# Performance work log

Hardware: AMD Instinct MI355X
Metric: run time of the kernel (lower is better)

The kernel has to match this reference:

```python
import jax, jax.numpy as jnp
import numpy as np

B, T, Nt = 64, 256, 77      # batch, motion length, text tokens
H, L = 8, 64                # num_heads, latent_dim per head
D = H * L                   # 512 model dim
Pt = 256                    # text_latent_dim
Ht = 1                      # num_text_heads
E, K = 8, 2                 # num_experts, topk
TEMB = 2048                 # time_embed_dim
MAXS, MAXTS = 512, 77       # max_seq_len, max_text_seq_len
NEG = -1e6


def _ln(x, g, b, eps=1e-5):
    m = jnp.mean(x, -1, keepdims=True)
    v = jnp.mean((x - m) ** 2, -1, keepdims=True)
    return (x - m) * jax.lax.rsqrt(v + eps) * g + b


def _gelu(x):
    return jax.nn.gelu(x, approximate=False)


def _moe_tokens(x, gate_w, fc1w, fc1b, fc2w, fc2b):
    # top-k softmax gate (fp32) + expert FFNs; dense compute, sparse combine.
    logits = x.astype(jnp.float32) @ gate_w.astype(jnp.float32)          # [Ntok,E]
    gates = jax.nn.softmax(logits, axis=-1)
    topv, topi = jax.lax.top_k(gates, K)
    topv = topv / jnp.sum(topv, -1, keepdims=True)
    dense = jnp.sum(jax.nn.one_hot(topi, E, dtype=topv.dtype) * topv[..., None], axis=1)
    dense = dense.astype(x.dtype)                                        # [Ntok,E]
    y = jnp.zeros((x.shape[0], fc2w.shape[-1]), x.dtype)
    for e in range(E):  # small fixed expert loop
        h = _gelu(x @ fc1w[e] + fc1b[e])
        y = y + dense[:, e:e + 1] * (h @ fc2w[e] + fc2b[e])
    return y


def _moe_block(x, pos, gate_w, fc1w, fc1b, fc2w, fc2b, projw, projb):
    # x: [B,Tn,Hn,Din]; add learned positional embedding, MoE over tokens, GELU, proj.
    b, t, h, d = x.shape
    x = x + pos[:, :t]
    y = _moe_tokens(x.reshape(-1, d), gate_w, fc1w, fc1b, fc2w, fc2b)
    y = _gelu(y) @ projw + projb
    return y.reshape(b, t, h, -1)


def _fwd(x, xf, emb, src_mask, norm_g, norm_b, tnorm_g, tnorm_b, m_pos, m_gate, m_fc1w, m_fc1b, m_fc2w, m_fc2b, m_projw, m_projb, t_pos, t_gate, t_fc1w, t_fc1b, t_fc2w, t_fc2b, t_projw, t_projb, body_w, sb_embw, sb_embb, sb_ng, sb_nb, sb_outw, sb_outb, cond_type):
    Bx, Tx, Dx = x.shape
    x4 = x.reshape(Bx, Tx, H, L)
    tf = xf.reshape(Bx, Nt, Ht, Pt)
    text_feat = _moe_block(_ln(tf, tnorm_g, tnorm_b), t_pos, t_gate, t_fc1w, t_fc1b, t_fc2w, t_fc2b, t_projw, t_projb)      # [B,Nt,Ht,2L]
    motion_feat = _moe_block(_ln(x4, norm_g, norm_b), m_pos, m_gate, m_fc1w, m_fc1b, m_fc2w, m_fc2b, m_projw, m_projb)      # [B,T,H,4L]
    # static body-part mixing
    bw = jax.nn.softmax(body_w, axis=1)
    body_feat = jnp.einsum('hl,bnld->bnhd', bw, motion_feat[..., :L]).reshape(Bx, Tx, Dx)
    tc = (cond_type % 10 > 0).astype(x.dtype).reshape(Bx, 1, 1, 1)
    sm = src_mask.reshape(Bx, Tx, 1, 1)
    key_text = jnp.broadcast_to(text_feat[..., :L] + (1.0 - tc) * NEG, (Bx, Nt, H, L))
    key_motion = motion_feat[..., L:2 * L] + (1.0 - sm) * NEG
    key = jax.nn.softmax(jnp.concatenate([key_text, key_motion], axis=1), axis=1)  # softmax over N
    val_text = jnp.broadcast_to(text_feat[..., L:] * tc, (Bx, Nt, H, L))
    val_motion = motion_feat[..., 2 * L:3 * L] * sm
    value = jnp.concatenate([val_text, val_motion], axis=1)                        # [B,N,H,L]
    query = jax.nn.softmax(motion_feat[..., 3 * L:], axis=-1)                      # [B,T,H,L]
    attn = jnp.einsum('bnhd,bnhl->bhdl', key, value)                               # [B,H,L,L]
    y_t = jnp.einsum('bnhd,bhdl->bnhl', query, attn).reshape(Bx, Tx, Dx)
    # StylizationBlock (eval: dropout is identity)
    h = _ln(body_feat + y_t, sb_ng, sb_nb)
    eo = jax.nn.silu(emb) @ sb_embw + sb_embb                                      # [B,2D]
    h = h * (1.0 + eo[:, None, :Dx]) + eo[:, None, Dx:]
    h = jax.nn.silu(h) @ sb_outw + sb_outb
    return x + h


def setup_inputs() -> dict:
    ks = iter(jax.random.split(jax.random.key(0), 48))
    nrm = lambda shape, s: jax.random.normal(next(ks), shape, jnp.float32) * s
    return {
        "x": nrm((B, T, D), 1.0),
        "xf": nrm((B, Nt, Pt), 1.0),
        "emb": nrm((B, TEMB), 1.0),
        "src_mask": jnp.ones((B, T, 1), jnp.float32),
        "norm_g": jnp.ones((L,), jnp.float32), "norm_b": jnp.zeros((L,), jnp.float32),
        "tnorm_g": jnp.ones((Pt,), jnp.float32), "tnorm_b": jnp.zeros((Pt,), jnp.float32),
        "m_pos": nrm((1, MAXS, H, L), 0.02),
        "m_gate": nrm((L, E), 0.02),
        "m_fc1w": nrm((E, L, 4 * L), 0.02), "m_fc1b": jnp.zeros((E, 4 * L), jnp.float32),
        "m_fc2w": nrm((E, 4 * L, L), 0.02), "m_fc2b": jnp.zeros((E, L), jnp.float32),
        "m_projw": nrm((L, 4 * L), 0.02), "m_projb": jnp.zeros((4 * L,), jnp.float32),
        "t_pos": nrm((1, MAXTS, Ht, Pt), 0.02),
        "t_gate": nrm((Pt, E), 0.02),
        "t_fc1w": nrm((E, Pt, 4 * Pt), 0.02), "t_fc1b": jnp.zeros((E, 4 * Pt), jnp.float32),
        "t_fc2w": nrm((E, 4 * Pt, Pt), 0.02), "t_fc2b": jnp.zeros((E, Pt), jnp.float32),
        "t_projw": nrm((Pt, 2 * L), 0.02), "t_projb": jnp.zeros((2 * L,), jnp.float32),
        "body_w": nrm((H, H), 1.0),
        "sb_embw": nrm((TEMB, 2 * D), 0.02), "sb_embb": jnp.zeros((2 * D,), jnp.float32),
        "sb_ng": jnp.ones((D,), jnp.float32), "sb_nb": jnp.zeros((D,), jnp.float32),
        "sb_outw": nrm((D, D), 0.02), "sb_outb": jnp.zeros((D,), jnp.float32),
        "cond_type": jax.random.randint(next(ks), (B, 1, 1), 0, 100, jnp.int32),
        "motion_length": T,
        "num_intervals": 1,
    }


def reference(x, xf, emb, src_mask, norm_g, norm_b, tnorm_g, tnorm_b, m_pos, m_gate, m_fc1w, m_fc1b, m_fc2w, m_fc2b, m_projw, m_projb, t_pos, t_gate, t_fc1w, t_fc1b, t_fc2w, t_fc2b, t_projw, t_projb, body_w, sb_embw, sb_embb, sb_ng, sb_nb, sb_outw, sb_outb, cond_type, motion_length, num_intervals):
    # motion_length / num_intervals are unused by the forward math (as in the source).
    return _fwd(x, xf, emb, src_mask, norm_g, norm_b, tnorm_g, tnorm_b, m_pos, m_gate, m_fc1w, m_fc1b, m_fc2w, m_fc2b, m_projw, m_projb, t_pos, t_gate, t_fc1w, t_fc1b, t_fc2w, t_fc2b, t_projw, t_projb, body_w, sb_embw, sb_embb, sb_ng, sb_nb, sb_outw, sb_outb, cond_type)
```

## Files before the change

### kernel.cpp

```cpp
#include <hip/hip_runtime.h>
#include <hip/hip_bf16.h>


typedef __hip_bfloat16 bf16;
typedef unsigned short u16;
typedef unsigned int   u32;
typedef __attribute__((ext_vector_type(8))) short short8;
typedef __attribute__((ext_vector_type(4))) short s16x4;
typedef __attribute__((ext_vector_type(4))) float f32x4;

#define MFMA16(a,b,c) __builtin_amdgcn_mfma_f32_16x16x32_bf16(a,b,c,0,0,0)

__device__ __forceinline__ float b2f(bf16 v){ return __bfloat162float(v); }
__device__ __forceinline__ u16 f2bu(float f){
  union { __hip_bfloat16 hh; u16 us; } cv; cv.hh = __float2bfloat16(f); return cv.us;
}
__device__ __forceinline__ float bu2f(u16 v){ return __uint_as_float(((u32)v)<<16); }

__device__ __forceinline__ float geluf(float x){
  float t = x*x;
  float w = x * fmaf(-0.10294453f, t, -2.3022077f);
  float z = exp2f(w);
  return x * __builtin_amdgcn_rcpf(1.f + z);
}
__device__ __forceinline__ float siluf(float x){
  float z = exp2f(-1.442695f * x);
  return x * __builtin_amdgcn_rcpf(1.f + z);
}

__device__ __forceinline__ float wsum(float v){
#pragma unroll
  for (int o=32;o>0;o>>=1) v += __shfl_xor(v,o,64);
  return v;
}
__device__ __forceinline__ float wmax(float v){
#pragma unroll
  for (int o=32;o>0;o>>=1) v = fmaxf(v, __shfl_xor(v,o,64));
  return v;
}
__device__ __forceinline__ void top2(const float* lg, int& i1, int& i2, float& wA){
  i1 = 0; float v1 = lg[0];
#pragma unroll
  for (int e=1;e<8;e++) if (lg[e] > v1){ v1 = lg[e]; i1 = e; }
  i2 = 0; float v2 = -1e30f;
#pragma unroll
  for (int e=0;e<8;e++) if (e != i1 && lg[e] > v2){ v2 = lg[e]; i2 = e; }
  wA = 1.f/(1.f + expf(v2 - v1));
}

__device__ __forceinline__ float sum2_wave(float x, int b0){
  float s = x, ss = x*x;
  float v = (b0 ? ss : s) + __shfl_xor(b0 ? s : ss, 1, 64);
  v += __shfl_xor(v, 2, 64);
  v += __shfl_xor(v, 4, 64);
  v += __shfl_xor(v, 8, 64);
  v += __shfl_xor(v, 16, 64);
  v += __shfl_xor(v, 32, 64);
  return v;
}

__device__ __forceinline__ float rsum8(const float p[8], int lane){
  int b0 = lane & 1, b1 = lane & 2, b2 = lane & 4;
  float w[4], u[2], v;
#pragma unroll
  for (int j=0;j<4;j++){
    float keep = b0 ? p[2*j+1] : p[2*j];
    float send = b0 ? p[2*j]   : p[2*j+1];
    w[j] = keep + __shfl_xor(send, 1, 64);
  }
#pragma unroll
// ... 90 lines not shown
  int tok = blockIdx.x, tid = threadIdx.x;
  int n = tok % 77;
  __shared__ float redw[32], lgs[8];
  int w = tid >> 6, ln = tid & 63;
  int b0 = tid & 1;
  float xv = xf[tok*256 + tid];
  float v = sum2_wave(xv, b0);
  if (ln < 2) redw[w*2 + ln] = v;
  __syncthreads();
  float mean = (redw[0]+redw[2]+redw[4]+redw[6]) * (1.f/256.f);
  float var  = (redw[1]+redw[3]+redw[5]+redw[7]) * (1.f/256.f) - mean*mean;
  float r = rsqrtf(var + 1e-5f);
  float xn = (xv - mean)*r*tg[tid] + tb[tid] + tpos[n*256 + tid];
  xtb[tok*256 + tid] = f2bu(xn);
  float p[8];
#pragma unroll
  for (int e=0;e<8;e++) p[e] = xn * gw[tid*8 + e];
  float vv = rsum8(p, ln);
  __syncthreads();
  if (ln < 8) redw[w*8 + ln] = vv;
  __syncthreads();
  if (tid < 8) lgs[tid] = redw[tid] + redw[8+tid] + redw[16+tid] + redw[24+tid];
  __syncthreads();
  if (tid == 0){
    int i1, i2; float wA; top2(lgs, i1, i2, wA);
    eidxT[tok] = make_int2(i1, i2);
    ewT[tok] = make_float2(wA, 1.f - wA);
  }
}

__global__ __launch_bounds__(256) void k_motion_pre(
    const float* __restrict__ x, const float* __restrict__ ng, const float* __restrict__ nb,
    const float* __restrict__ mpos, const float* __restrict__ gw,
    u16* __restrict__ xmb, int2* __restrict__ eidxM, float2* __restrict__ ewM){
  int tok = blockIdx.x*4 + (threadIdx.x >> 6);
  int d = threadIdx.x & 63;
  int b0 = d & 1;
  float xv = x[(size_t)tok*64 + d];
  float v = sum2_wave(xv, b0);
  float o = __shfl_xor(v, 1, 64);
  float sf  = b0 ? o : v;
  float ssf = b0 ? v : o;
  float mean = sf * (1.f/64.f);
  float var  = ssf * (1.f/64.f) - mean*mean;
  float r = rsqrtf(var + 1e-5f);
  int h = tok & 7; int t = (tok >> 3) & 255;
  float xn = (xv - mean)*r*ng[d] + nb[d] + mpos[(t*8+h)*64 + d];
  xmb[(size_t)tok*64 + d] = f2bu(xn);
  float p[8];
#pragma unroll
  for (int e=0;e<8;e++) p[e] = xn * gw[d*8 + e];
  float vv = rsum8(p, d);
  float lg[8];
#pragma unroll
  for (int e=0;e<8;e++) lg[e] = __shfl(vv, e, 64);
  if (d == 0){
    int i1, i2; float wA; top2(lg, i1, i2, wA);
    eidxM[tok] = make_int2(i1, i2);
    ewM[tok] = make_float2(wA, 1.f - wA);
  }
}

__global__ __launch_bounds__(256, 4) void k_motion_moe(
    const u16* __restrict__ xmb, const int* __restrict__ alistM, const int* __restrict__ cnts,
    const u16* __restrict__ w1pk, const float* __restrict__ fc1b,
    const u16* __restrict__ w2pk, const float* __restrict__ fc2b,
    u16* __restrict__ ycM){
  int e = blockIdx.y, tile = blockIdx.x, tid = threadIdx.x;
  int cnt = cnts[8+e]; int base = tile*32;
  if (base >= cnt) return;
  int nn = min(32, cnt - base); int off = e*131072;
  __shared__ int toks[32];
  __shared__ u16 xs[32*72];
  __shared__ u16 hT[32*264];
  if (tid < 32) toks[tid] = alistM[off + base + min(tid, nn-1)];
  __syncthreads();
  { int row = tid >> 3, c0 = (tid & 7)*8;
    short8 v = *(const short8*)(xmb + (size_t)(toks[row]>>1)*64 + c0);
    *(short8*)&xs[row*72 + c0] = v; }
  __syncthreads();
  int lane = tid & 63, w = tid >> 6;
  int n = lane & 15, q = lane >> 4;
  int mt = w & 1;
  short8 x0 = *(const short8*)&xs[(mt*16 + n)*72 + q*8];
  short8 x1 = *(const short8*)&xs[(mt*16 + n)*72 + 32 + q*8];
  const short8* b1 = (const short8*)(w1pk + (size_t)e*16384);
  short8 b1f[16];
#pragma unroll
  for (int i=0;i<8;i++){
    int nt = (w>>1)*8 + i;
    b1f[2*i]   = b1[(nt*2+0)*64 + lane];
    b1f[2*i+1] = b1[(nt*2+1)*64 + lane];
  }
#pragma unroll
  for (int i=0;i<8;i++){
    int nt = (w>>1)*8 + i;
    f32x4 acc = {0.f,0.f,0.f,0.f};
    acc = MFMA16(b1f[2*i],   x0, acc);
    acc = MFMA16(b1f[2*i+1], x1, acc);
    f32x4 bias = *(const f32x4*)(fc1b + e*256 + nt*16 + q*4);
    s16x4 o;
#pragma unroll
    for (int r=0;r<4;r++) o[r] = (short)f2bu(geluf(acc[r] + bias[r]));
    *(s16x4*)&hT[(mt*16 + n)*264 + nt*16 + q*4] = o;
  }
  __syncthreads();
  short8 a2[8];
#pragma unroll
  for (int kc=0;kc<8;kc++) a2[kc] = *(const short8*)&hT[(mt*16 + n)*264 + kc*32 + q*8];
  const short8* b2 = (const short8*)(w2pk + (size_t)e*16384);
  bool valid = (mt*16 + n) < nn;
  int slot = toks[mt*16 + n];
#pragma unroll
  for (int i=0;i<2;i++){
    int nt = (w>>1)*2 + i;
    f32x4 acc = {0.f,0.f,0.f,0.f};
#pragma unroll
    for (int kc=0;kc<8;kc++) acc = MFMA16(b2[(nt*8+kc)*64 + lane], a2[kc], acc);
    f32x4 bias = *(const f32x4*)(fc2b + e*64 + nt*16 + q*4);
    if (valid){
      s16x4 o;
#pragma unroll
      for (int r=0;r<4;r++) o[r] = (short)f2bu(acc[r] + bias[r]);
      *(s16x4*)(ycM + (size_t)slot*64 + nt*16 + q*4) = o;
    }
  }
}

__global__ __launch_bounds__(256) void k_text_moe(
    const u16* __restrict__ xtb, const int* __restrict__ alistT, const int* __restrict__ cnts,
    const u16* __restrict__ w1pk, const float* __restrict__ fc1b,
    const u16* __restrict__ w2pk, const float* __restrict__ fc2b,
    float* __restrict__ ycT){
  int e = blockIdx.y, tile = blockIdx.x, tid = threadIdx.x;
  int cnt = cnts[e]; int base = tile*16;
  if (base >= cnt) return;
  int nn = min(16, cnt - base); int off = e*4928;
  __shared__ int toks[16];
  __shared__ u16 xs[16*280];
  __shared__ u16 hT[16*1048];
  if (tid < 16) toks[tid] = alistT[off + base + min(tid, nn-1)];
  __syncthreads();
  { int row = tid >> 4, c0 = (tid & 15)*16;
    const short8* sp = (const short8*)(xtb + (size_t)(toks[row]>>1)*256 + c0);
    short8 v0 = sp[0], v1 = sp[1];
    *(short8*)&xs[row*280 + c0] = v0;
    *(short8*)&xs[row*280 + c0 + 8] = v1; }
  __syncthreads();
  int lane = tid & 63, w = tid >> 6;
  int n = lane & 15, q = lane >> 4;
  short8 a_[8];
#pragma unroll
  for (int kc=0;kc<8;kc++) a_[kc] = *(const short8*)&xs[n*280 + kc*32 + q*8];
  const short8* b1 = (const short8*)(w1pk + (size_t)e*262144);
#pragma unroll 1
  for (int i=0;i<16;i++){
    int nt = w*16 + i;
// ... 16 lines not shown
#pragma unroll
    for (int i=0;i<4;i++){
      int nt = w*4 + i;
      acc[i] = MFMA16(a, b2[(nt*32+kc)*64 + lane], acc[i]);
    }
  }
#pragma unroll
  for (int i=0;i<4;i++){
    int nt = w*4 + i;
    float bias = fc2b[e*256 + nt*16 + n];
#pragma unroll
    for (int r=0;r<4;r++){
      int row = q*4 + r;
      if (row < nn) ycT[(size_t)toks[row]*256 + nt*16 + n] = acc[i][r] + bias;
    }
  }
}

__global__ __launch_bounds__(128) void k_text_combine(
    const float* __restrict__ ycT, const float2* __restrict__ ewT,
    const float* __restrict__ pw, const float* __restrict__ pb,
    float* __restrict__ tfeat){
  int t = blockIdx.x, tid = threadIdx.x;
  __shared__ float gy[256];
  float2 w = ewT[t];
  for (int c=tid; c<256; c+=128){
    float y = w.x*ycT[(size_t)(t*2)*256 + c] + w.y*ycT[(size_t)(t*2+1)*256 + c];
    gy[c] = geluf(y);
  }
  __syncthreads();
  float a = pb[tid];
  for (int k=0;k<256;k++) a += gy[k] * pw[k*128 + tid];
  tfeat[(size_t)t*128 + tid] = a;
}

__global__ __launch_bounds__(256) void k_mproj(
    const u16* __restrict__ ycM, const float2* __restrict__ ewM,
    const u16* __restrict__ wpk, const float* __restrict__ pb,
    u16* __restrict__ mf, u16* __restrict__ qs){
  int t0 = blockIdx.x*32, tid = threadIdx.x;
  __shared__ u16 xs[32*72];
  { int row = tid >> 3, c0 = (tid & 7)*8;
    int tok = t0 + row;
    float2 wgt = ewM[tok];
    short8 v0 = *(const short8*)(ycM + (size_t)(tok*2)*64 + c0);
    short8 v1 = *(const short8*)(ycM + (size_t)(tok*2+1)*64 + c0);
    short8 o;
#pragma unroll
    for (int j=0;j<8;j++)
      o[j] = (short)f2bu(geluf(wgt.x*bu2f((u16)v0[j]) + wgt.y*bu2f((u16)v1[j])));
    *(short8*)&xs[row*72 + c0] = o; }
  __syncthreads();
  int lane = tid & 63, w = tid >> 6;
  int n = lane & 15, q = lane >> 4;
  int mt = w & 1;
  short8 a0 = *(const short8*)&xs[(mt*16 + n)*72 + q*8];
  short8 a1 = *(const short8*)&xs[(mt*16 + n)*72 + 32 + q*8];
  const short8* bp = (const short8*)wpk;
  float vals[4][4];
#pragma unroll
  for (int i=0;i<8;i++){
    int nt = (w>>1)*8 + i;
    f32x4 acc = {0.f,0.f,0.f,0.f};
    acc = MFMA16(a0, bp[(nt*2+0)*64 + lane], acc);
    acc = MFMA16(a1, bp[(nt*2+1)*64 + lane], acc);
    float bias = pb[nt*16 + n];
#pragma unroll
    for (int r=0;r<4;r++){
      float v = acc[r] + bias;
      if (w >= 2 && i >= 4) vals[i-4][r] = v;
      int tok = t0 + mt*16 + q*4 + r;
      mf[(size_t)tok*256 + nt*16 + n] = f2bu(v);
    }
  }
  if (w >= 2){
#pragma unroll
    for (int r=0;r<4;r++){
      int tok = t0 + mt*16 + q*4 + r;
      float m = fmaxf(fmaxf(vals[0][r], vals[1][r]), fmaxf(vals[2][r], vals[3][r]));
#pragma unroll
      for (int o=8;o>0;o>>=1) m = fmaxf(m, __shfl_xor(m, o, 64));
      float e0 = expf(vals[0][r]-m), e1 = expf(vals[1][r]-m);
      float e2 = expf(vals[2][r]-m), e3 = expf(vals[3][r]-m);
      float s = (e0+e1) + (e2+e3);
#pragma unroll
      for (int o=8;o>0;o>>=1) s += __shfl_xor(s, o, 64);
      float inv = __builtin_amdgcn_rcpf(s);
      u16* qp = qs + (size_t)tok*64 + n;
      qp[0]  = f2bu(e0*inv);
      qp[16] = f2bu(e1*inv);
      qp[32] = f2bu(e2*inv);
      qp[48] = f2bu(e3*inv);
    }
  }
}

__global__ __launch_bounds__(256) void k_eo1(const float* __restrict__ emb, const float* __restrict__ ew,
                      float* __restrict__ ep){
  int ct = blockIdx.x & 15;
  int ks = blockIdx.x >> 4;
  int tid = threadIdx.x;
  int k0 = ks*128, c0 = ct*64;
  __shared__ float aS[128*68];
  __shared__ float bS[128*64];
#pragma unroll
  for (int i=0;i<8;i++){
    int idx4 = tid + i*256;
    int b = idx4 >> 5, kq = idx4 & 31;
    f32x4 v = *(const f32x4*)(emb + (size_t)b*2048 + k0 + kq*4);
    aS[(kq*4+0)*68 + b] = siluf(v[0]);
    aS[(kq*4+1)*68 + b] = siluf(v[1]);
    aS[(kq*4+2)*68 + b] = siluf(v[2]);
    aS[(kq*4+3)*68 + b] = siluf(v[3]);
  }
#pragma unroll
  for (int i=0;i<8;i++){
    int idx4 = tid + i*256;
    int kk = idx4 >> 4, cq = idx4 & 15;
    *(f32x4*)&bS[kk*64 + cq*4] = *(const f32x4*)(ew + (size_t)(k0+kk)*1024 + c0 + cq*4);
  }
  __syncthreads();
  int cg = tid & 15, bg = tid >> 4;
  f32x4 acc[4] = {{0.f,0.f,0.f,0.f},{0.f,0.f,0.f,0.f},{0.f,0.f,0.f,0.f},{0.f,0.f,0.f,0.f}};
#pragma unroll 4
  for (int kk=0;kk<128;kk++){
    f32x4 a = *(const f32x4*)&aS[kk*68 + bg*4];
    f32x4 bb = *(const f32x4*)&bS[kk*64 + cg*4];
#pragma unroll
    for (int i=0;i<4;i++){
      acc[i][0] += a[i]*bb[0];
      acc[i][1] += a[i]*bb[1];
      acc[i][2] += a[i]*bb[2];
      acc[i][3] += a[i]*bb[3];
    }
  }
#pragma unroll
  for (int i=0;i<4;i++){
    int b = bg*4 + i;
    *(f32x4*)&ep[((size_t)(ks*64 + b))*1024 + c0 + cg*4] = acc[i];
  }
}

__global__ __launch_bounds__(256) void k_eo2(const float* __restrict__ ep, const float* __restrict__ ebias,
                      float* __restrict__ eo){
  int idx = blockIdx.x*256 + threadIdx.x;
  int c = idx & 1023;
  float s = ebias[c];
#pragma unroll
  for (int ks=0;ks<16;ks++) s += ep[(size_t)ks*65536 + idx];
  eo[idx] = s;
}

#define AT_STRIDE 364
__global__ __launch_bounds__(512) void k_attn(const float* __restrict__ tfeat, const u16* __restrict__ mf,
                       const float* __restrict__ src_mask, const int* __restrict__ cond,
                       u16* __restrict__ attnT){
  int b = blockIdx.x >> 3; int h = blockIdx.x & 7;
  int tid = threadIdx.x; int c = tid & 63; int part = tid >> 6;
  __shared__ u16 ebT[64*AT_STRIDE];
  __shared__ u16 vbT[64*AT_STRIDE];
  __shared__ float colmax[64], colsum[64], red[512];
  float tc = ((cond[b] % 10) > 0) ? 1.f : 0.f;
  float negt = (1.f - tc) * (-1e6f);

  float mx = -1e30f;
  for (int k = 0; k < 11; k++){
    int n0 = part*44 + k*4;
    s16x4 kb4, vb4;
#pragma unroll
    for (int jj = 0; jj < 4; jj++){
      int n = n0 + jj;
      float kv, vv;
      if (n < 77){
        const float* trow = tfeat + (b*77+n)*128;
        kv = trow[c] + negt;
        vv = trow[64 + c] * tc;
      } else if (n < 333){
        int t = n - 77; float smv = src_mask[b*256 + t];
        const u16* mrow = mf + ((size_t)(b*256+t)*8+h)*256;
        kv = bu2f(mrow[64 + c]) + (1.f - smv)*(-1e6f);
        vv = bu2f(mrow[128 + c]) * smv;
      } else { kv = -1e30f; vv = 0.f; }
      kb4[jj] = (short)f2bu(kv);
      vb4[jj] = (short)f2bu(vv);
      mx = fmaxf(mx, kv);
    }
    *(s16x4*)&ebT[c*AT_STRIDE + n0] = kb4;
    *(s16x4*)&vbT[c*AT_STRIDE + n0] = vb4;
  }
// ... 19 lines not shown
      s16x4 o;
      o[0]=(short)f2bu(e0); o[1]=(short)f2bu(e1); o[2]=(short)f2bu(e2); o[3]=(short)f2bu(e3);
      *(s16x4*)&ebT[rowc*AT_STRIDE + n0] = o;
    }
    red[tid] = s;
  }
  __syncthreads();
  if (tid < 64){
    float t2 = 0.f;
#pragma unroll
    for (int p=0;p<8;p++) t2 += red[tid*8 + p];
    colsum[tid] = t2;
  }
  __syncthreads();
  int lane = tid & 63, w = tid >> 6;
  int n16 = lane & 15, q = lane >> 4;
  int mt = w >> 1;
  int ntb = (w & 1) * 2;
  f32x4 acc0 = {0.f,0.f,0.f,0.f}, acc1 = {0.f,0.f,0.f,0.f};
  const u16* ea = &ebT[(mt*16 + n16)*AT_STRIDE + q*8];
  const u16* v0p = &vbT[(ntb*16 + n16)*AT_STRIDE + q*8];
  const u16* v1p = &vbT[((ntb+1)*16 + n16)*AT_STRIDE + q*8];
#pragma unroll
  for (int kc = 0; kc < 11; kc++){
    short8 a  = ld8(ea  + kc*32);
    short8 b0 = ld8(v0p + kc*32);
    short8 b1 = ld8(v1p + kc*32);
    acc0 = MFMA16(a, b0, acc0);
    acc1 = MFMA16(a, b1, acc1);
  }
  float inv[4];
#pragma unroll
  for (int r=0;r<4;r++) inv[r] = __builtin_amdgcn_rcpf(colsum[mt*16 + q*4 + r]);
  u16* outp = attnT + (size_t)(b*8+h)*4096;
  int d0 = mt*16 + q*4;
  {
    int l = ntb*16 + n16;
    s16x4 o;
#pragma unroll
    for (int r=0;r<4;r++) o[r] = (short)f2bu(acc0[r]*inv[r]);
    *(s16x4*)(outp + l*64 + d0) = o;
  }
  {
    int l = (ntb+1)*16 + n16;
    s16x4 o;
#pragma unroll
    for (int r=0;r<4;r++) o[r] = (short)f2bu(acc1[r]*inv[r]);
    *(s16x4*)(outp + l*64 + d0) = o;
  }
}

__global__ __launch_bounds__(256) void k_yt(const u16* __restrict__ qs, const u16* __restrict__ attnT,
                                            u16* __restrict__ yt){
  int b = blockIdx.x >> 3; int h = blockIdx.x & 7;
  int tid = threadIdx.x;
  int lane = tid & 63, w = tid >> 6;
  int n = lane & 15, q = lane >> 4;
  const u16* qsb = qs + ((size_t)(b*256)*8 + h)*64;
  const u16* ab  = attnT + (size_t)(b*8+h)*4096;
  f32x4 acc[4][4];
#pragma unroll
  for (int mt=0;mt<4;mt++)
#pragma unroll
    for (int nt=0;nt<4;nt++) acc[mt][nt] = (f32x4){0.f,0.f,0.f,0.f};
#pragma unroll
  for (int kc=0;kc<2;kc++){
    short8 a_[4], b_[4];
#pragma unroll
    for (int mt=0;mt<4;mt++){
      int t = w*64 + mt*16 + n;
      a_[mt] = *(const short8*)(qsb + (size_t)t*512 + kc*32 + q*8);
    }
#pragma unroll
    for (int nt=0;nt<4;nt++){
      int l = nt*16 + n;
      b_[nt] = *(const short8*)(ab + l*64 + kc*32 + q*8);
    }
#pragma unroll
    for (int mt=0;mt<4;mt++)
#pragma unroll
      for (int nt=0;nt<4;nt++)
        acc[mt][nt] = MFMA16(a_[mt], b_[nt], acc[mt][nt]);
  }
#pragma unroll
  for (int mt=0;mt<4;mt++)
#pragma unroll
    for (int nt=0;nt<4;nt++){
      int l = nt*16 + n;
#pragma unroll
      for (int r=0;r<4;r++){
        int t = w*64 + mt*16 + q*4 + r;
        yt[((size_t)(b*256+t)*8 + h)*64 + l] = f2bu(acc[mt][nt][r]);
      }
    }
}

__global__ __launch_bounds__(256) void k_j2(const u16* __restrict__ mf, const u16* __restrict__ yt,
                     const float* __restrict__ bwv, const float* __restrict__ eo,
                     const float* __restrict__ sb_ng, const float* __restrict__ sb_nb,
                     float* __restrict__ sbuf){
  int blk = blockIdx.x; int b = blk >> 8; int t = blk & 255;
  int tid = threadIdx.x;
  __shared__ float mfl[512], red[4];
#pragma unroll
  for (int ii=0; ii<2; ii++){
    int idx = tid + ii*256; int h = idx >> 6; int dd = idx & 63;
    mfl[idx] = bu2f(mf[((size_t)(b*256+t)*8+h)*256 + dd]);
  }
  __syncthreads();
  int w = tid >> 6, ln = tid & 63;
  float out[2];
#pragma unroll
  for (int ii=0; ii<2; ii++){
    int idx = tid + ii*256; int h = idx >> 6; int l = idx & 63;
    float a = bu2f(yt[((size_t)(b*256+t)*8 + h)*64 + l]);
    float bs = 0.f;
#pragma unroll
    for (int lh=0; lh<8; lh++) bs += bwv[h*8 + lh] * mfl[lh*64 + l];
    out[ii] = a + bs;
  }
  float psum = wsum(out[0] + out[1]);
  if (ln == 0) red[w] = psum;
  __syncthreads();
  float mean = (red[0]+red[1]+red[2]+red[3]) * (1.f/512.f);
  __syncthreads();
  float c0 = out[0]-mean, c1 = out[1]-mean;
  float pv = wsum(c0*c0 + c1*c1);
  if (ln == 0) red[w] = pv;
  __syncthreads();
  float var = (red[0]+red[1]+red[2]+red[3]) * (1.f/512.f);
  float r = rsqrtf(var + 1e-5f);
#pragma unroll
  for (int ii=0; ii<2; ii++){
    int c = tid + ii*256;
    float hn = (out[ii]-mean)*r*sb_ng[c] + sb_nb[c];
    float e1 = eo[b*1024 + c], e2 = eo[b*1024 + 512 + c];
    float hm = hn*(1.f + e1) + e2;
    sbuf[(size_t)blk*512 + c] = siluf(hm);
  }
}

__global__ __launch_bounds__(256) void k_out(const u16* __restrict__ wpk,
                      const float* __restrict__ bias, const float* __restrict__ x,
                      float* __restrict__ out){
  int r0 = blockIdx.x*32, tid = threadIdx.x;
  __shared__ u16 xs[32*536];
  { int row = tid >> 3, c0 = (tid & 7)*64;
    const f32x4* sp = (const f32x4*)(out + (size_t)(r0+row)*512 + c0);
#pragma unroll
    for (int j=0;j<8;j++){
      f32x4 va = sp[2*j], vb = sp[2*j+1];
      short8 o;
      o[0]=(short)f2bu(va[0]); o[1]=(short)f2bu(va[1]); o[2]=(short)f2bu(va[2]); o[3]=(short)f2bu(va[3]);
      o[4]=(short)f2bu(vb[0]); o[5]=(short)f2bu(vb[1]); o[6]=(short)f2bu(vb[2]); o[7]=(short)f2bu(vb[3]);
      *(short8*)&xs[row*536 + c0 + 8*j] = o;
    } }
  __syncthreads();
  int lane = tid & 63, w = tid >> 6;
  int n = lane & 15, q = lane >> 4;
  int mt = w & 1;
  short8 a_[16];
#pragma unroll
  for (int kc=0;kc<16;kc++) a_[kc] = *(const short8*)&xs[(mt*16 + n)*536 + kc*32 + q*8];
  const short8* bp = (const short8*)wpk;
#pragma unroll 1
  for (int i=0;i<16;i++){
    int nt = (w>>1)*16 + i;
    f32x4 acc = {0.f,0.f,0.f,0.f};
#pragma unroll
    for (int kc=0;kc<16;kc++) acc = MFMA16(a_[kc], bp[(nt*16+kc)*64 + lane], acc);
    int col = nt*16 + n;
    float bv = bias[col];
#pragma unroll
    for (int r=0;r<4;r++){
      size_t rowg = (size_t)(r0 + mt*16 + q*4 + r);
      out[rowg*512 + col] = acc[r] + bv + x[rowg*512 + col];
    }
  }
}

extern "C" void kernel_launch(void* const* d_in, const int* in_sizes, int n_in,
                              void* d_out, int out_size, void* d_ws, size_t ws_size,
                              hipStream_t stream) {
  (void)in_sizes; (void)n_in; (void)out_size; (void)ws_size;
  const float* x        = (const float*)d_in[0];
  const float* xf       = (const float*)d_in[1];
  const float* emb      = (const float*)d_in[2];
  const float* src_mask = (const float*)d_in[3];
  const float* norm_g   = (const float*)d_in[4];
// ... 3 lines not shown
  const float* m_pos    = (const float*)d_in[8];
  const float* m_gate   = (const float*)d_in[9];
  const float* m_fc1w   = (const float*)d_in[10];
  const float* m_fc1b   = (const float*)d_in[11];
  const float* m_fc2w   = (const float*)d_in[12];
  const float* m_fc2b   = (const float*)d_in[13];
  const float* m_projw  = (const float*)d_in[14];
  const float* m_projb  = (const float*)d_in[15];
  const float* t_pos    = (const float*)d_in[16];
  const float* t_gate   = (const float*)d_in[17];
  const float* t_fc1w   = (const float*)d_in[18];
  const float* t_fc1b   = (const float*)d_in[19];
  const float* t_fc2w   = (const float*)d_in[20];
  const float* t_fc2b   = (const float*)d_in[21];
  const float* t_projw  = (const float*)d_in[22];
  const float* t_projb  = (const float*)d_in[23];
  const float* body_w   = (const float*)d_in[24];
  const float* sb_embw  = (const float*)d_in[25];
  const float* sb_embb  = (const float*)d_in[26];
  const float* sb_ng    = (const float*)d_in[27];
  const float* sb_nb    = (const float*)d_in[28];
  const float* sb_outw  = (const float*)d_in[29];
  const float* sb_outb  = (const float*)d_in[30];
  const int*   cond     = (const int*)d_in[31];

  char* base = (char*)d_ws;
  size_t o = 0;
  auto alloc = [&](size_t bytes)->char*{ char* r = base + o; o += (bytes + 255) & ~(size_t)255; return r; };
  u16*  mf      = (u16*)alloc(67108864);
  char* R       = alloc(33554432);
  float* ep     = (float*)(R);
  u16*  xtb     = (u16*)(R);
  float* ycT    = (float*)(R + 4194304);
  u16*  ycM     = (u16*)(R);
  u16*  attnT   = (u16*)(R);
  u16*  yt      = (u16*)(R + 8388608);
  u16*  xmb     = (u16*)alloc(16777216);
  u16*  qs      = xmb;
  u16*  t1pk    = (u16*)alloc(4194304);
  u16*  t2pk    = (u16*)alloc(4194304);
  u16*  m1pk    = (u16*)alloc(262144);
  u16*  m2pk    = (u16*)alloc(262144);
  u16*  mppk    = (u16*)alloc(32768);
  u16*  wopk    = (u16*)alloc(524288);
  int2* eidxT   = (int2*)alloc(39424);
  float2* ewT   = (float2*)alloc(39424);
  int2* eidxM   = (int2*)alloc(1048576);
  float2* ewM   = (float2*)alloc(1048576);
  int*  alistT  = (int*)alloc(157696);
  int*  alistM  = (int*)alloc(4194304);
  int*  cnts    = (int*)alloc(256);
  float* tfeat  = (float*)alloc(2523136);
  float* eo     = (float*)alloc(262144);
  float* bwv    = (float*)alloc(256);
  float* sbuf   = (float*)d_out;

  k_init<<<1, 64, 0, stream>>>(cnts, body_w, bwv);
  k_repack_all<<<18496, 256, 0, stream>>>(t_fc1w, t1pk, t_fc2w, t2pk, m_fc1w, m1pk,
                                          m_fc2w, m2pk, m_projw, mppk, sb_outw, wopk);
  k_eo1<<<256, 256, 0, stream>>>(emb, sb_embw, ep);
  k_eo2<<<256, 256, 0, stream>>>(ep, sb_embb, eo);

  k_text_pre<<<4928, 256, 0, stream>>>(xf, tnorm_g, tnorm_b, t_pos, t_gate, xtb, eidxT, ewT);
  k_motion_pre<<<32768, 256, 0, stream>>>(x, norm_g, norm_b, m_pos, m_gate, xmb, eidxM, ewM);
  k_filld<<<32, 256, 0, stream>>>(eidxT, 4928, 4928, cnts, alistT);
  k_filld<<<256, 256, 0, stream>>>(eidxM, 131072, 131072, cnts + 8, alistM);

  k_text_moe<<<dim3(308, 8), 256, 0, stream>>>(xtb, alistT, cnts, t1pk, t_fc1b, t2pk, t_fc2b, ycT);
  k_text_combine<<<4928, 128, 0, stream>>>(ycT, ewT, t_projw, t_projb, tfeat);

  k_motion_moe<<<dim3(4096, 8), 256, 0, stream>>>(xmb, alistM, cnts, m1pk, m_fc1b, m2pk, m_fc2b, ycM);
  k_mproj<<<4096, 256, 0, stream>>>(ycM, ewM, mppk, m_projb, mf, qs);

  k_attn<<<512, 512, 0, stream>>>(tfeat, mf, src_mask, cond, attnT);
  k_yt<<<512, 256, 0, stream>>>(qs, attnT, yt);
  k_j2<<<16384, 256, 0, stream>>>(mf, yt, bwv, eo, sb_ng, sb_nb, sbuf);
  k_out<<<512, 256, 0, stream>>>(wopk, sb_outb, x, (float*)d_out);
}
```

Baseline: 477.2 us.

## Compute motion MoE densely over all experts and fuse projection and softmax

Replaces the routed motion MoE (token lists, per-expert tiles, intermediate per-slot outputs) with a dense kernel that runs all eight experts per 32-token tile. It weights each expert by a dense per-token gate vector and then applies GELU, the projection and the softmax in the same kernel. This removes the list-building launch, the gather and the round-trip of the intermediate expert outputs through global memory. The cost is four times more expert matmul work, since non-selected experts are computed with zero weight.

```diff
diff --git a/kernel.cpp b/kernel.cpp
--- a/kernel.cpp
+++ b/kernel.cpp
@@ -31,11 +31,6 @@
 __device__ __forceinline__ float wsum(float v){
 #pragma unroll
   for (int o=32;o>0;o>>=1) v += __shfl_xor(v,o,64);
-  return v;
-}
-__device__ __forceinline__ float wmax(float v){
-#pragma unroll
-  for (int o=32;o>0;o>>=1) v = fmaxf(v, __shfl_xor(v,o,64));
   return v;
 }
 __device__ __forceinline__ void top2(const float* lg, int& i1, int& i2, float& wA){
@@ -192,7 +187,7 @@
 __global__ __launch_bounds__(256) void k_motion_pre(
     const float* __restrict__ x, const float* __restrict__ ng, const float* __restrict__ nb,
     const float* __restrict__ mpos, const float* __restrict__ gw,
-    u16* __restrict__ xmb, int2* __restrict__ eidxM, float2* __restrict__ ewM){
+    u16* __restrict__ xmb, float* __restrict__ w8){
   int tok = blockIdx.x*4 + (threadIdx.x >> 6);
   int d = threadIdx.x & 63;
   int b0 = d & 1;
@@ -214,75 +209,122 @@
   float lg[8];
 #pragma unroll
   for (int e=0;e<8;e++) lg[e] = __shfl(vv, e, 64);
-  if (d == 0){
+  if (d < 8){
     int i1, i2; float wA; top2(lg, i1, i2, wA);
-    eidxM[tok] = make_int2(i1, i2);
-    ewM[tok] = make_float2(wA, 1.f - wA);
-  }
-}
-
-__global__ __launch_bounds__(256, 4) void k_motion_moe(
-    const u16* __restrict__ xmb, const int* __restrict__ alistM, const int* __restrict__ cnts,
+    float wv = (d == i1) ? wA : ((d == i2) ? (1.f - wA) : 0.f);
+    w8[(size_t)tok*8 + d] = wv;
+  }
+}
+
+__global__ __launch_bounds__(256, 4) void k_motion_dense(
+    const u16* __restrict__ xmb, const float* __restrict__ w8,
     const u16* __restrict__ w1pk, const float* __restrict__ fc1b,
     const u16* __restrict__ w2pk, const float* __restrict__ fc2b,
-    u16* __restrict__ ycM){
-  int e = blockIdx.y, tile = blockIdx.x, tid = threadIdx.x;
-  int cnt = cnts[8+e]; int base = tile*32;
-  if (base >= cnt) return;
-  int nn = min(32, cnt - base); int off = e*131072;
-  __shared__ int toks[32];
+    const u16* __restrict__ wppk, const float* __restrict__ pb,
+    u16* __restrict__ mf, u16* __restrict__ qs){
+  int t0 = blockIdx.x*32, tid = threadIdx.x;
+  __shared__ u16 hT[2][32*264];
   __shared__ u16 xs[32*72];
-  __shared__ u16 hT[32*264];
-  if (tid < 32) toks[tid] = alistM[off + base + min(tid, nn-1)];
-  __syncthreads();
+  __shared__ float ws[256];
   { int row = tid >> 3, c0 = (tid & 7)*8;
-    short8 v = *(const short8*)(xmb + (size_t)(toks[row]>>1)*64 + c0);
-    *(short8*)&xs[row*72 + c0] = v; }
+    *(short8*)&xs[row*72 + c0] = *(const short8*)(xmb + (size_t)(t0+row)*64 + c0); }
+  ws[tid] = w8[(size_t)t0*8 + tid];
   __syncthreads();
   int lane = tid & 63, w = tid >> 6;
   int n = lane & 15, q = lane >> 4;
-  int mt = w & 1;
-  short8 x0 = *(const short8*)&xs[(mt*16 + n)*72 + q*8];
-  short8 x1 = *(const short8*)&xs[(mt*16 + n)*72 + 32 + q*8];
-  const short8* b1 = (const short8*)(w1pk + (size_t)e*16384);
-  short8 b1f[16];
-#pragma unroll
-  for (int i=0;i<8;i++){
-    int nt = (w>>1)*8 + i;
-    b1f[2*i]   = b1[(nt*2+0)*64 + lane];
-    b1f[2*i+1] = b1[(nt*2+1)*64 + lane];
-  }
-#pragma unroll
-  for (int i=0;i<8;i++){
-    int nt = (w>>1)*8 + i;
+  int mt = w & 1, wp = w >> 1;
+  int tok = mt*16 + n;
+  short8 x0 = *(const short8*)&xs[tok*72 + q*8];
+  short8 x1 = *(const short8*)&xs[tok*72 + 32 + q*8];
+  float yacc[2][4];
+#pragma unroll
+  for (int i=0;i<2;i++)
+#pragma unroll
+    for (int r=0;r<4;r++) yacc[i][r] = 0.f;
+#pragma unroll 1
+  for (int e=0;e<8;e++){
+    u16* hb = hT[e & 1];
+    const short8* b1 = (const short8*)(w1pk + (size_t)e*16384);
+#pragma unroll
+    for (int i=0;i<8;i++){
+      int nt = wp*8 + i;
+      f32x4 acc = {0.f,0.f,0.f,0.f};
+      acc = MFMA16(b1[(nt*2+0)*64 + lane], x0, acc);
+      acc = MFMA16(b1[(nt*2+1)*64 + lane], x1, acc);
+      f32x4 bias = *(const f32x4*)(fc1b + e*256 + nt*16 + q*4);
+      s16x4 o;
+#pragma unroll
+      for (int r=0;r<4;r++) o[r] = (short)f2bu(geluf(acc[r] + bias[r]));
+      *(s16x4*)&hb[tok*264 + nt*16 + q*4] = o;
+    }
+    __syncthreads();
+    short8 a2[8];
+#pragma unroll
+    for (int kc=0;kc<8;kc++) a2[kc] = ld8(&hb[tok*264 + kc*32 + q*8]);
+    const short8* b2 = (const short8*)(w2pk + (size_t)e*16384);
+    float we = ws[tok*8 + e];
+#pragma unroll
+    for (int i=0;i<2;i++){
+      int nt = wp*2 + i;
+      f32x4 acc = {0.f,0.f,0.f,0.f};
+#pragma unroll
+      for (int kc=0;kc<8;kc++) acc = MFMA16(b2[(nt*8+kc)*64 + lane], a2[kc], acc);
+      f32x4 bias = *(const f32x4*)(fc2b + e*64 + nt*16 + q*4);
+#pragma unroll
+      for (int r=0;r<4;r++) yacc[i][r] += we * (acc[r] + bias[r]);
+    }
+  }
+#pragma unroll
+  for (int i=0;i<2;i++){
+    int ch0 = (wp*2 + i)*16 + q*4;
+    s16x4 o;
+#pragma unroll
+    for (int r=0;r<4;r++) o[r] = (short)f2bu(geluf(yacc[i][r]));
+    *(s16x4*)&xs[tok*72 + ch0] = o;
+  }
+  __syncthreads();
+  short8 bx0 = *(const short8*)&xs[tok*72 + q*8];
+  short8 bx1 = *(const short8*)&xs[tok*72 + 32 + q*8];
+  const short8* bp = (const short8*)wppk;
+  float vals[4][4];
+#pragma unroll
+  for (int i8=0;i8<8;i8++){
+    int i = wp*8 + i8;
     f32x4 acc = {0.f,0.f,0.f,0.f};
-    acc = MFMA16(b1f[2*i],   x0, acc);
-    acc = MFMA16(b1f[2*i+1], x1, acc);
-    f32x4 bias = *(const f32x4*)(fc1b + e*256 + nt*16 + q*4);
+    acc = MFMA16(bp[(i*2+0)*64 + lane], bx0, acc);
+    acc = MFMA16(bp[(i*2+1)*64 + lane], bx1, acc);
+    f32x4 bias = *(const f32x4*)(pb + i*16 + q*4);
     s16x4 o;
 #pragma unroll
-    for (int r=0;r<4;r++) o[r] = (short)f2bu(geluf(acc[r] + bias[r]));
-    *(s16x4*)&hT[(mt*16 + n)*264 + nt*16 + q*4] = o;
-  }
-  __syncthreads();
-  short8 a2[8];
-#pragma unroll
-  for (int kc=0;kc<8;kc++) a2[kc] = *(const short8*)&hT[(mt*16 + n)*264 + kc*32 + q*8];
-  const short8* b2 = (const short8*)(w2pk + (size_t)e*16384);
-  bool valid = (mt*16 + n) < nn;
-  int slot = toks[mt*16 + n];
-#pragma unroll
-  for (int i=0;i<2;i++){
-    int nt = (w>>1)*2 + i;
-    f32x4 acc = {0.f,0.f,0.f,0.f};
-#pragma unroll
-    for (int kc=0;kc<8;kc++) acc = MFMA16(b2[(nt*8+kc)*64 + lane], a2[kc], acc);
-    f32x4 bias = *(const f32x4*)(fc2b + e*64 + nt*16 + q*4);
-    if (valid){
+    for (int r=0;r<4;r++){
+      float v = acc[r] + bias[r];
+      if (wp == 1 && i8 >= 4) vals[i8-4][r] = v;
+      o[r] = (short)f2bu(v);
+    }
+    *(s16x4*)(mf + (size_t)(t0+tok)*256 + i*16 + q*4) = o;
+  }
+  if (wp == 1){
+    float m = -1e30f;
+#pragma unroll
+    for (int j=0;j<4;j++)
+#pragma unroll
+      for (int r=0;r<4;r++) m = fmaxf(m, vals[j][r]);
+    m = fmaxf(m, __shfl_xor(m, 16, 64));
+    m = fmaxf(m, __shfl_xor(m, 32, 64));
+    float ev[4][4]; float s = 0.f;
+#pragma unroll
+    for (int j=0;j<4;j++)
+#pragma unroll
+      for (int r=0;r<4;r++){ ev[j][r] = expf(vals[j][r] - m); s += ev[j][r]; }
+    s += __shfl_xor(s, 16, 64);
+    s += __shfl_xor(s, 32, 64);
+    float inv = __builtin_amdgcn_rcpf(s);
+#pragma unroll
+    for (int j=0;j<4;j++){
       s16x4 o;
 #pragma unroll
-      for (int r=0;r<4;r++) o[r] = (short)f2bu(acc[r] + bias[r]);
-      *(s16x4*)(ycM + (size_t)slot*64 + nt*16 + q*4) = o;
+      for (int r=0;r<4;r++) o[r] = (short)f2bu(ev[j][r]*inv);
+      *(s16x4*)(qs + (size_t)(t0+tok)*64 + j*16 + q*4) = o;
     }
   }
 }
@@ -365,67 +407,6 @@
   float a = pb[tid];
   for (int k=0;k<256;k++) a += gy[k] * pw[k*128 + tid];
   tfeat[(size_t)t*128 + tid] = a;
-}
-
-__global__ __launch_bounds__(256) void k_mproj(
-    const u16* __restrict__ ycM, const float2* __restrict__ ewM,
-    const u16* __restrict__ wpk, const float* __restrict__ pb,
-    u16* __restrict__ mf, u16* __restrict__ qs){
-  int t0 = blockIdx.x*32, tid = threadIdx.x;
-  __shared__ u16 xs[32*72];
-  { int row = tid >> 3, c0 = (tid & 7)*8;
-    int tok = t0 + row;
-    float2 wgt = ewM[tok];
-    short8 v0 = *(const short8*)(ycM + (size_t)(tok*2)*64 + c0);
-    short8 v1 = *(const short8*)(ycM + (size_t)(tok*2+1)*64 + c0);
-    short8 o;
-#pragma unroll
-    for (int j=0;j<8;j++)
-      o[j] = (short)f2bu(geluf(wgt.x*bu2f((u16)v0[j]) + wgt.y*bu2f((u16)v1[j])));
-    *(short8*)&xs[row*72 + c0] = o; }
-  __syncthreads();
-  int lane = tid & 63, w = tid >> 6;
-  int n = lane & 15, q = lane >> 4;
-  int mt = w & 1;
-  short8 a0 = *(const short8*)&xs[(mt*16 + n)*72 + q*8];
-  short8 a1 = *(const short8*)&xs[(mt*16 + n)*72 + 32 + q*8];
-  const short8* bp = (const short8*)wpk;
-  float vals[4][4];
-#pragma unroll
-  for (int i=0;i<8;i++){
-    int nt = (w>>1)*8 + i;
-    f32x4 acc = {0.f,0.f,0.f,0.f};
-    acc = MFMA16(a0, bp[(nt*2+0)*64 + lane], acc);
-    acc = MFMA16(a1, bp[(nt*2+1)*64 + lane], acc);
-    float bias = pb[nt*16 + n];
-#pragma unroll
-    for (int r=0;r<4;r++){
-      float v = acc[r] + bias;
-      if (w >= 2 && i >= 4) vals[i-4][r] = v;
-      int tok = t0 + mt*16 + q*4 + r;
-      mf[(size_t)tok*256 + nt*16 + n] = f2bu(v);
-    }
-  }
-  if (w >= 2){
-#pragma unroll
-    for (int r=0;r<4;r++){
-      int tok = t0 + mt*16 + q*4 + r;
-      float m = fmaxf(fmaxf(vals[0][r], vals[1][r]), fmaxf(vals[2][r], vals[3][r]));
-#pragma unroll
-      for (int o=8;o>0;o>>=1) m = fmaxf(m, __shfl_xor(m, o, 64));
-      float e0 = expf(vals[0][r]-m), e1 = expf(vals[1][r]-m);
-      float e2 = expf(vals[2][r]-m), e3 = expf(vals[3][r]-m);
-      float s = (e0+e1) + (e2+e3);
-#pragma unroll
-      for (int o=8;o>0;o>>=1) s += __shfl_xor(s, o, 64);
-      float inv = __builtin_amdgcn_rcpf(s);
-      u16* qp = qs + (size_t)tok*64 + n;
-      qp[0]  = f2bu(e0*inv);
-      qp[16] = f2bu(e1*inv);
-      qp[32] = f2bu(e2*inv);
-      qp[48] = f2bu(e3*inv);
-    }
-  }
 }
 
 __global__ __launch_bounds__(256) void k_eo1(const float* __restrict__ emb, const float* __restrict__ ew,
@@ -765,7 +746,6 @@
   float* ep     = (float*)(R);
   u16*  xtb     = (u16*)(R);
   float* ycT    = (float*)(R + 4194304);
-  u16*  ycM     = (u16*)(R);
   u16*  attnT   = (u16*)(R);
   u16*  yt      = (u16*)(R + 8388608);
   u16*  xmb     = (u16*)alloc(16777216);
@@ -778,10 +758,8 @@
   u16*  wopk    = (u16*)alloc(524288);
   int2* eidxT   = (int2*)alloc(39424);
   float2* ewT   = (float2*)alloc(39424);
-  int2* eidxM   = (int2*)alloc(1048576);
-  float2* ewM   = (float2*)alloc(1048576);
+  float* w8     = (float*)alloc(4194304);
   int*  alistT  = (int*)alloc(157696);
-  int*  alistM  = (int*)alloc(4194304);
   int*  cnts    = (int*)alloc(256);
   float* tfeat  = (float*)alloc(2523136);
   float* eo     = (float*)alloc(262144);
@@ -795,15 +773,14 @@
   k_eo2<<<256, 256, 0, stream>>>(ep, sb_embb, eo);
 
   k_text_pre<<<4928, 256, 0, stream>>>(xf, tnorm_g, tnorm_b, t_pos, t_gate, xtb, eidxT, ewT);
-  k_motion_pre<<<32768, 256, 0, stream>>>(x, norm_g, norm_b, m_pos, m_gate, xmb, eidxM, ewM);
+  k_motion_pre<<<32768, 256, 0, stream>>>(x, norm_g, norm_b, m_pos, m_gate, xmb, w8);
   k_filld<<<32, 256, 0, stream>>>(eidxT, 4928, 4928, cnts, alistT);
-  k_filld<<<256, 256, 0, stream>>>(eidxM, 131072, 131072, cnts + 8, alistM);
 
   k_text_moe<<<dim3(308, 8), 256, 0, stream>>>(xtb, alistT, cnts, t1pk, t_fc1b, t2pk, t_fc2b, ycT);
   k_text_combine<<<4928, 128, 0, stream>>>(ycT, ewT, t_projw, t_projb, tfeat);
 
-  k_motion_moe<<<dim3(4096, 8), 256, 0, stream>>>(xmb, alistM, cnts, m1pk, m_fc1b, m2pk, m_fc2b, ycM);
-  k_mproj<<<4096, 256, 0, stream>>>(ycM, ewM, mppk, m_projb, mf, qs);
+  k_motion_dense<<<4096, 256, 0, stream>>>(xmb, w8, m1pk, m_fc1b, m2pk, m_fc2b,
+                                           mppk, m_projb, mf, qs);
 
   k_attn<<<512, 512, 0, stream>>>(tfeat, mf, src_mask, cond, attnT);
   k_yt<<<512, 256, 0, stream>>>(qs, attnT, yt);
```

Result: slower. 658.4 us (+38.0%).

## Fuse attention output GEMM into k_attn and fold LayerNorm/modulation into k_out

Applied to the files above, without the earlier changes.

The attention kernel now stages its normalized attention matrix in shared memory and immediately multiplies it by the query slice to produce yt. This removes the separate k_yt launch and the global round trip of attnT. The per-row body mixing, LayerNorm, time-embedding modulation and SiLU previously done in k_j2 (16384 blocks writing fp32 to the output buffer) are folded into k_out's prologue. That prologue writes bf16 straight into the shared tile used by the output GEMM. This removes an fp32 write and read of the full activation tensor plus two launches, but variance is now computed in one pass as E[x²]−mean², which is less numerically robust.

```diff
diff --git a/kernel.cpp b/kernel.cpp
--- a/kernel.cpp
+++ b/kernel.cpp
@@ -31,11 +31,6 @@
 __device__ __forceinline__ float wsum(float v){
 #pragma unroll
   for (int o=32;o>0;o>>=1) v += __shfl_xor(v,o,64);
-  return v;
-}
-__device__ __forceinline__ float wmax(float v){
-#pragma unroll
-  for (int o=32;o>0;o>>=1) v = fmaxf(v, __shfl_xor(v,o,64));
   return v;
 }
 __device__ __forceinline__ void top2(const float* lg, int& i1, int& i2, float& wA){
@@ -485,9 +480,10 @@
 }
 
 #define AT_STRIDE 364
+#define AS_STRIDE 76
 __global__ __launch_bounds__(512) void k_attn(const float* __restrict__ tfeat, const u16* __restrict__ mf,
                        const float* __restrict__ src_mask, const int* __restrict__ cond,
-                       u16* __restrict__ attnT){
+                       const u16* __restrict__ qs, u16* __restrict__ yt){
   int b = blockIdx.x >> 3; int h = blockIdx.x & 7;
   int tid = threadIdx.x; int c = tid & 63; int part = tid >> 6;
   __shared__ u16 ebT[64*AT_STRIDE];
@@ -573,129 +569,111 @@
   float inv[4];
 #pragma unroll
   for (int r=0;r<4;r++) inv[r] = __builtin_amdgcn_rcpf(colsum[mt*16 + q*4 + r]);
-  u16* outp = attnT + (size_t)(b*8+h)*4096;
-  int d0 = mt*16 + q*4;
+  __syncthreads();
+  u16* attnS = ebT;
   {
-    int l = ntb*16 + n16;
-    s16x4 o;
-#pragma unroll
-    for (int r=0;r<4;r++) o[r] = (short)f2bu(acc0[r]*inv[r]);
-    *(s16x4*)(outp + l*64 + d0) = o;
-  }
-  {
-    int l = (ntb+1)*16 + n16;
-    s16x4 o;
-#pragma unroll
-    for (int r=0;r<4;r++) o[r] = (short)f2bu(acc1[r]*inv[r]);
-    *(s16x4*)(outp + l*64 + d0) = o;
-  }
-}
-
-__global__ __launch_bounds__(256) void k_yt(const u16* __restrict__ qs, const u16* __restrict__ attnT,
-                                            u16* __restrict__ yt){
-  int b = blockIdx.x >> 3; int h = blockIdx.x & 7;
-  int tid = threadIdx.x;
-  int lane = tid & 63, w = tid >> 6;
-  int n = lane & 15, q = lane >> 4;
+    int d0 = mt*16 + q*4;
+    int l0 = ntb*16 + n16, l1 = (ntb+1)*16 + n16;
+    s16x4 o0, o1;
+#pragma unroll
+    for (int r=0;r<4;r++){ o0[r] = (short)f2bu(acc0[r]*inv[r]); o1[r] = (short)f2bu(acc1[r]*inv[r]); }
+    *(s16x4*)&attnS[l0*AS_STRIDE + d0] = o0;
+    *(s16x4*)&attnS[l1*AS_STRIDE + d0] = o1;
+  }
+  __syncthreads();
   const u16* qsb = qs + ((size_t)(b*256)*8 + h)*64;
-  const u16* ab  = attnT + (size_t)(b*8+h)*4096;
-  f32x4 acc[4][4];
-#pragma unroll
-  for (int mt=0;mt<4;mt++)
-#pragma unroll
-    for (int nt=0;nt<4;nt++) acc[mt][nt] = (f32x4){0.f,0.f,0.f,0.f};
+  f32x4 ya[2][4];
+#pragma unroll
+  for (int m2=0;m2<2;m2++)
+#pragma unroll
+    for (int nt=0;nt<4;nt++) ya[m2][nt] = (f32x4){0.f,0.f,0.f,0.f};
 #pragma unroll
   for (int kc=0;kc<2;kc++){
-    short8 a_[4], b_[4];
-#pragma unroll
-    for (int mt=0;mt<4;mt++){
-      int t = w*64 + mt*16 + n;
-      a_[mt] = *(const short8*)(qsb + (size_t)t*512 + kc*32 + q*8);
-    }
+    short8 a0 = *(const short8*)(qsb + (size_t)(w*32 + n16)*512 + kc*32 + q*8);
+    short8 a1 = *(const short8*)(qsb + (size_t)(w*32 + 16 + n16)*512 + kc*32 + q*8);
+    short8 b_[4];
+#pragma unroll
+    for (int nt=0;nt<4;nt++) b_[nt] = ld8(&attnS[(nt*16 + n16)*AS_STRIDE + kc*32 + q*8]);
 #pragma unroll
     for (int nt=0;nt<4;nt++){
-      int l = nt*16 + n;
-      b_[nt] = *(const short8*)(ab + l*64 + kc*32 + q*8);
-    }
-#pragma unroll
-    for (int mt=0;mt<4;mt++)
-#pragma unroll
-      for (int nt=0;nt<4;nt++)
-        acc[mt][nt] = MFMA16(a_[mt], b_[nt], acc[mt][nt]);
-  }
-#pragma unroll
-  for (int mt=0;mt<4;mt++)
+      ya[0][nt] = MFMA16(a0, b_[nt], ya[0][nt]);
+      ya[1][nt] = MFMA16(a1, b_[nt], ya[1][nt]);
+    }
+  }
+#pragma unroll
+  for (int m2=0;m2<2;m2++)
 #pragma unroll
     for (int nt=0;nt<4;nt++){
-      int l = nt*16 + n;
+      int l = nt*16 + n16;
 #pragma unroll
       for (int r=0;r<4;r++){
-        int t = w*64 + mt*16 + q*4 + r;
-        yt[((size_t)(b*256+t)*8 + h)*64 + l] = f2bu(acc[mt][nt][r]);
+        int t = w*32 + m2*16 + q*4 + r;
+        yt[((size_t)(b*256+t)*8 + h)*64 + l] = f2bu(ya[m2][nt][r]);
       }
     }
-}
-
-__global__ __launch_bounds__(256) void k_j2(const u16* __restrict__ mf, const u16* __restrict__ yt,
-                     const float* __restrict__ bwv, const float* __restrict__ eo,
-                     const float* __restrict__ sb_ng, const float* __restrict__ sb_nb,
-                     float* __restrict__ sbuf){
-  int blk = blockIdx.x; int b = blk >> 8; int t = blk & 255;
-  int tid = threadIdx.x;
-  __shared__ float mfl[512], red[4];
-#pragma unroll
-  for (int ii=0; ii<2; ii++){
-    int idx = tid + ii*256; int h = idx >> 6; int dd = idx & 63;
-    mfl[idx] = bu2f(mf[((size_t)(b*256+t)*8+h)*256 + dd]);
-  }
-  __syncthreads();
-  int w = tid >> 6, ln = tid & 63;
-  float out[2];
-#pragma unroll
-  for (int ii=0; ii<2; ii++){
-    int idx = tid + ii*256; int h = idx >> 6; int l = idx & 63;
-    float a = bu2f(yt[((size_t)(b*256+t)*8 + h)*64 + l]);
-    float bs = 0.f;
-#pragma unroll
-    for (int lh=0; lh<8; lh++) bs += bwv[h*8 + lh] * mfl[lh*64 + l];
-    out[ii] = a + bs;
-  }
-  float psum = wsum(out[0] + out[1]);
-  if (ln == 0) red[w] = psum;
-  __syncthreads();
-  float mean = (red[0]+red[1]+red[2]+red[3]) * (1.f/512.f);
-  __syncthreads();
-  float c0 = out[0]-mean, c1 = out[1]-mean;
-  float pv = wsum(c0*c0 + c1*c1);
-  if (ln == 0) red[w] = pv;
-  __syncthreads();
-  float var = (red[0]+red[1]+red[2]+red[3]) * (1.f/512.f);
-  float r = rsqrtf(var + 1e-5f);
-#pragma unroll
-  for (int ii=0; ii<2; ii++){
-    int c = tid + ii*256;
-    float hn = (out[ii]-mean)*r*sb_ng[c] + sb_nb[c];
-    float e1 = eo[b*1024 + c], e2 = eo[b*1024 + 512 + c];
-    float hm = hn*(1.f + e1) + e2;
-    sbuf[(size_t)blk*512 + c] = siluf(hm);
-  }
 }
 
 __global__ __launch_bounds__(256) void k_out(const u16* __restrict__ wpk,
                       const float* __restrict__ bias, const float* __restrict__ x,
+                      const u16* __restrict__ mf, const u16* __restrict__ yt,
+                      const float* __restrict__ bwv, const float* __restrict__ eo,
+                      const float* __restrict__ sb_ng, const float* __restrict__ sb_nb,
                       float* __restrict__ out){
   int r0 = blockIdx.x*32, tid = threadIdx.x;
+  int b = r0 >> 8;
   __shared__ u16 xs[32*536];
-  { int row = tid >> 3, c0 = (tid & 7)*64;
-    const f32x4* sp = (const f32x4*)(out + (size_t)(r0+row)*512 + c0);
-#pragma unroll
-    for (int j=0;j<8;j++){
-      f32x4 va = sp[2*j], vb = sp[2*j+1];
-      short8 o;
-      o[0]=(short)f2bu(va[0]); o[1]=(short)f2bu(va[1]); o[2]=(short)f2bu(va[2]); o[3]=(short)f2bu(va[3]);
-      o[4]=(short)f2bu(vb[0]); o[5]=(short)f2bu(vb[1]); o[6]=(short)f2bu(vb[2]); o[7]=(short)f2bu(vb[3]);
-      *(short8*)&xs[row*536 + c0 + 8*j] = o;
-    } }
+  __shared__ u16 mfl[32*520];
+#pragma unroll
+  for (int i=0;i<8;i++){
+    int idx = tid + i*256;
+    int rw = idx >> 6, rem = idx & 63;
+    int hh = rem >> 3, d0 = (rem & 7)*8;
+    *(short8*)&mfl[rw*520 + hh*64 + d0] =
+      *(const short8*)(mf + (((size_t)(r0+rw)*8 + hh)*256) + d0);
+  }
+  __syncthreads();
+  {
+    int row = tid >> 3, hh = tid & 7;
+    float bw8[8];
+#pragma unroll
+    for (int lh=0;lh<8;lh++) bw8[lh] = bwv[hh*8 + lh];
+    const u16* ytrow = yt + (((size_t)(r0+row)*8 + hh)*64);
+    float out64[64];
+    float s1 = 0.f, s2 = 0.f;
+#pragma unroll
+    for (int lc=0;lc<8;lc++){
+      short8 yv = *(const short8*)(ytrow + lc*8);
+      float o[8];
+#pragma unroll
+      for (int j=0;j<8;j++) o[j] = bu2f((u16)yv[j]);
+#pragma unroll
+      for (int lh=0;lh<8;lh++){
+        short8 m = *(const short8*)&mfl[row*520 + lh*64 + lc*8];
+#pragma unroll
+        for (int j=0;j<8;j++) o[j] = fmaf(bw8[lh], bu2f((u16)m[j]), o[j]);
+      }
+#pragma unroll
+      for (int j=0;j<8;j++){ out64[lc*8+j] = o[j]; s1 += o[j]; s2 += o[j]*o[j]; }
+    }
+    s1 += __shfl_xor(s1, 1, 64); s2 += __shfl_xor(s2, 1, 64);
+    s1 += __shfl_xor(s1, 2, 64); s2 += __shfl_xor(s2, 2, 64);
+    s1 += __shfl_xor(s1, 4, 64); s2 += __shfl_xor(s2, 4, 64);
+    float mean = s1 * (1.f/512.f);
+    float var  = s2 * (1.f/512.f) - mean*mean;
+    float rr = rsqrtf(var + 1e-5f);
+#pragma unroll
+    for (int lc=0;lc<8;lc++){
+      short8 o8;
+#pragma unroll
+      for (int j=0;j<8;j++){
+        int cch = hh*64 + lc*8 + j;
+        float hn = (out64[lc*8+j]-mean)*rr*sb_ng[cch] + sb_nb[cch];
+        float hm = hn*(1.f + eo[b*1024 + cch]) + eo[b*1024 + 512 + cch];
+        o8[j] = (short)f2bu(siluf(hm));
+      }
+      *(short8*)&xs[row*536 + hh*64 + lc*8] = o8;
+    }
+  }
   __syncthreads();
   int lane = tid & 63, w = tid >> 6;
   int n = lane & 15, q = lane >> 4;
@@ -766,7 +744,6 @@
   u16*  xtb     = (u16*)(R);
   float* ycT    = (float*)(R + 4194304);
   u16*  ycM     = (u16*)(R);
-  u16*  attnT   = (u16*)(R);
   u16*  yt      = (u16*)(R + 8388608);
   u16*  xmb     = (u16*)alloc(16777216);
   u16*  qs      = xmb;
@@ -786,7 +763,6 @@
   float* tfeat  = (float*)alloc(2523136);
   float* eo     = (float*)alloc(262144);
   float* bwv    = (float*)alloc(256);
-  float* sbuf   = (float*)d_out;
 
   k_init<<<1, 64, 0, stream>>>(cnts, body_w, bwv);
   k_repack_all<<<18496, 256, 0, stream>>>(t_fc1w, t1pk, t_fc2w, t2pk, m_fc1w, m1pk,
@@ -805,8 +781,6 @@
   k_motion_moe<<<dim3(4096, 8), 256, 0, stream>>>(xmb, alistM, cnts, m1pk, m_fc1b, m2pk, m_fc2b, ycM);
   k_mproj<<<4096, 256, 0, stream>>>(ycM, ewM, mppk, m_projb, mf, qs);
 
-  k_attn<<<512, 512, 0, stream>>>(tfeat, mf, src_mask, cond, attnT);
-  k_yt<<<512, 256, 0, stream>>>(qs, attnT, yt);
-  k_j2<<<16384, 256, 0, stream>>>(mf, yt, bwv, eo, sb_ng, sb_nb, sbuf);
-  k_out<<<512, 256, 0, stream>>>(wopk, sb_outb, x, (float*)d_out);
-}
+  k_attn<<<512, 512, 0, stream>>>(tfeat, mf, src_mask, cond, qs, yt);
+  k_out<<<512, 256, 0, stream>>>(wopk, sb_outb, x, mf, yt, bwv, eo, sb_ng, sb_nb, (float*)d_out);
+}
```

Result: no change. 475.3 us (-0.4%).
